# Kernel tuning notes

Measured on AMD Instinct MI355X. Metric: run time of the kernel, lower is better.

The kernel has to match this reference:

```python
import jax, jax.numpy as jnp
import numpy as np

B, N, C = 16, 2048, 512
NUM_HEADS = 8
D = C // NUM_HEADS  # 64


def setup_inputs() -> dict:
    key = jax.random.key(0)
    ks = jax.random.split(key, 8)
    s = 0.02
    return {
        "x": jax.random.normal(ks[0], (B, N, C), dtype=jnp.float32),
        "Wq": jax.random.normal(ks[1], (D, C), dtype=jnp.float32) * s,
        "bq": jax.random.normal(ks[2], (D,), dtype=jnp.float32) * s,
        "Wk": jax.random.normal(ks[3], (D, C), dtype=jnp.float32) * s,
        "bk": jax.random.normal(ks[4], (D,), dtype=jnp.float32) * s,
        "Wv": jax.random.normal(ks[5], (C, C), dtype=jnp.float32) * s,
        "bv": jax.random.normal(ks[6], (C,), dtype=jnp.float32) * s,
        "gamma": jax.random.normal(ks[7], (1,), dtype=jnp.float32) * 0.1,
    }


def reference(x, Wq, bq, Wk, bk, Wv, bv, gamma):
    # x: [B, N, C]; torch code permutes to [B, C, N] (channels for Conv1d)
    xt = jnp.transpose(x, (0, 2, 1))                      # [B, C, N]
    # 1x1 Conv1d == pointwise linear over channel dim
    q = jnp.einsum('dc,bcn->bdn', Wq, xt) + bq[None, :, None]   # [B, D, N]
    k = jnp.einsum('dc,bcn->bdn', Wk, xt) + bk[None, :, None]   # [B, D, N]
    v = jnp.einsum('oc,bcn->bon', Wv, xt) + bv[None, :, None]   # [B, C, N]
    # energy[b, n, m] = <q[:, n], k[:, m]>
    energy = jnp.einsum('bdn,bdm->bnm', q, k)             # [B, N, N]
    attention = jax.nn.softmax(energy, axis=-1)           # [B, N, N]
    # out = bmm(v, attention^T): out[b, c, n] = sum_m v[b, c, m] * attn[b, n, m]
    out = jnp.einsum('bcm,bnm->bcn', v, attention)        # [B, C, N]
    out = gamma[0] * out + xt
    return jnp.transpose(out, (0, 2, 1))                  # [B, N, C]
```

## Files before the change

### kernel.cpp

```cpp
#include <hip/hip_runtime.h>
#include <hip/hip_bf16.h>

typedef __bf16 bf16x8 __attribute__((ext_vector_type(8)));
typedef float f32x4 __attribute__((ext_vector_type(4)));

#define B_ 16
#define N_ 2048
#define C_ 512
#define D_ 64

__device__ __forceinline__ float bf2f(ushort u) {
    union { uint i; float f; } w; w.i = ((uint)u) << 16; return w.f;
}
__device__ __forceinline__ ushort f2bf(float f) {
    union { float f; uint i; } w; w.f = f;
    uint u = w.i;
    u = (u + 0x7fffu + ((u >> 16) & 1u)) >> 16;
    return (ushort)u;
}
__device__ __forceinline__ __bf16 u2b(ushort u) {
    union { ushort s; __bf16 b; } w; w.s = u; return w.b;
}
__device__ __forceinline__ bf16x8 ld8u(const ushort* p) { return *(const bf16x8*)p; }
__device__ __forceinline__ bf16x8 ld8f(const float* p) {
    f32x4 a = *(const f32x4*)p;
    f32x4 b = *(const f32x4*)(p + 4);
    bf16x8 r;
    r[0] = u2b(f2bf(a[0])); r[1] = u2b(f2bf(a[1]));
    r[2] = u2b(f2bf(a[2])); r[3] = u2b(f2bf(a[3]));
    r[4] = u2b(f2bf(b[0])); r[5] = u2b(f2bf(b[1]));
    r[6] = u2b(f2bf(b[2])); r[7] = u2b(f2bf(b[3]));
    return r;
}

__device__ __forceinline__ void gload16(const ushort* g, ushort* l) {
    __builtin_amdgcn_global_load_lds(
        (const __attribute__((address_space(1))) void*)g,
        (__attribute__((address_space(3))) void*)l, 16, 0, 0);
}

__global__ void probe_kernel(const void* x, int* flag) {
    int lane = threadIdx.x & 63;
    ushort u = ((const ushort*)x)[lane * 2];
    float v = fabsf(bf2f(u));
    bool sane = (v > 9.3e-10f) && (v < 1.1e9f) && (v == v);
    unsigned long long m = __ballot(sane);
    if (threadIdx.x == 0) *flag = (__popcll(m) >= 48) ? 0 : 1;
}

__launch_bounds__(256, 2)
__global__ void proj_all(const void* __restrict__ X,
                         const void* __restrict__ Wq_, const void* __restrict__ bq_,
                         const void* __restrict__ Wk_, const void* __restrict__ bk_,
                         const void* __restrict__ Wv_, const void* __restrict__ bv_,
                         ushort* __restrict__ outq,
                         ushort* __restrict__ outk,
                         ushort* __restrict__ outv,
                         const int* __restrict__ flag) {
    const int isf32 = *flag;
    __shared__ ushort lA[128][72];
    __shared__ ushort lB[128][72];
    const int tid  = threadIdx.x;
    const int wave = tid >> 6, lane = tid & 63;
    const int quad = lane >> 4, li = lane & 15;
    const int wr = (wave & 1) * 64;
    const int wc = (wave >> 1) * 64;
    const int m0 = blockIdx.x * 128;
    const int n0 = blockIdx.y * 128;

    f32x4 acc[4][4];
    #pragma unroll
    for (int i = 0; i < 4; ++i)
        #pragma unroll
        for (int j = 0; j < 4; ++j) acc[i][j] = (f32x4){0.f, 0.f, 0.f, 0.f};

    for (int k0 = 0; k0 < C_; k0 += 64) {
        __syncthreads();
        #pragma unroll
        for (int it = 0; it < 4; ++it) {
            int idx = tid + it * 256;
            int row = idx >> 3, seg = idx & 7;
            int n = n0 + row;
            size_t ea = (size_t)(m0 + row) * C_ + k0 + seg * 8;
            if (!isf32) {
                const ushort* bs = (n < 64)  ? (const ushort*)Wq_ + (size_t)n * C_
                                 : (n < 128) ? (const ushort*)Wk_ + (size_t)(n - 64) * C_
                                             : (const ushort*)Wv_ + (size_t)(n - 128) * C_;
                *(bf16x8*)&lA[row][seg * 8] = ld8u((const ushort*)X + ea);
                *(bf16x8*)&lB[row][seg * 8] = ld8u(bs + k0 + seg * 8);
            } else {
                const float* bs = (n < 64)  ? (const float*)Wq_ + (size_t)n * C_
                                : (n < 128) ? (const float*)Wk_ + (size_t)(n - 64) * C_
                                            : (const float*)Wv_ + (size_t)(n - 128) * C_;
                *(bf16x8*)&lA[row][seg * 8] = ld8f((const float*)X + ea);
                *(bf16x8*)&lB[row][seg * 8] = ld8f(bs + k0 + seg * 8);
            }
        }
        __syncthreads();
        #pragma unroll
        for (int ks = 0; ks < 2; ++ks) {
            bf16x8 af[4], bfr[4];
            #pragma unroll
            for (int i = 0; i < 4; ++i)
                af[i] = *(const bf16x8*)&lA[wr + i * 16 + li][ks * 32 + quad * 8];
            #pragma unroll
            for (int j = 0; j < 4; ++j)
                bfr[j] = *(const bf16x8*)&lB[wc + j * 16 + li][ks * 32 + quad * 8];
            #pragma unroll
            for (int i = 0; i < 4; ++i)
                #pragma unroll
                for (int j = 0; j < 4; ++j)
                    acc[i][j] = __builtin_amdgcn_mfma_f32_16x16x32_bf16(
                        af[i], bfr[j], acc[i][j], 0, 0, 0);
        }
    }

    #pragma unroll
    for (int j2 = 0; j2 < 4; ++j2) {
        int c = n0 + wc + j2 * 16 + li;
        float bv;
        if (!isf32) {
            bv = (c < 64)  ? bf2f(((const ushort*)bq_)[c])
               : (c < 128) ? bf2f(((const ushort*)bk_)[c - 64])
                           : bf2f(((const ushort*)bv_)[c - 128]);
        } else {
            bv = (c < 64)  ? ((const float*)bq_)[c]
               : (c < 128) ? ((const float*)bk_)[c - 64]
                           : ((const float*)bv_)[c - 128];
        }
        if (c < 128) {
            ushort* dst = (c < 64) ? outq : outk;
            int cl = c & 63;
            #pragma unroll
            for (int i = 0; i < 4; ++i)
                #pragma unroll
                for (int j = 0; j < 4; ++j) {
                    int m = m0 + wr + i * 16 + quad * 4 + j;
                    dst[(size_t)m * D_ + cl] = f2bf(acc[i][j2][j] + bv);
                }
        } else {
            int cv = c - 128;
            #pragma unroll
            for (int i = 0; i < 4; ++i) {
                int m = m0 + wr + i * 16 + quad * 4;
                int b = m >> 11, ml = m & (N_ - 1);
                ushort4 pk;
                pk.x = f2bf(acc[i][j2][0] + bv);
                pk.y = f2bf(acc[i][j2][1] + bv);
                pk.z = f2bf(acc[i][j2][2] + bv);
                pk.w = f2bf(acc[i][j2][3] + bv);
                *(ushort4*)(outv + ((size_t)(b * C_ + cv)) * N_ + ml) = pk;
            }
        }
    }
}

__launch_bounds__(512, 4)
__global__ void attn_fused(const ushort* __restrict__ q,
                           const ushort* __restrict__ kk,
                           const ushort* __restrict__ vt,
                           const void* __restrict__ x,
                           const void* __restrict__ gptr,
                           void* __restrict__ out,
                           const int* __restrict__ flag) {
    __shared__ ushort Vl[2][256 * 64];
    __shared__ ushort Pl[64 * 64];
    __shared__ float  ll[64];

    const int tid  = threadIdx.x;
    const int wave = tid >> 6, lane = tid & 63;
    const int quad = lane >> 4, li = lane & 15;
    const int wq = wave & 1;
    const int wm = wave >> 1;
    const int b  = blockIdx.z;
    const int q0 = blockIdx.x * 64;
    const int c0 = blockIdx.y * 256;

    const ushort* kb = kk + (size_t)b * N_ * D_;
    const ushort* vb = vt + ((size_t)b * C_ + c0) * N_;

    const int lrow8 = lane >> 3;
    const int lseg  = (lane & 7) ^ lrow8;

    bf16x8 qf[2][2];
    #pragma unroll
    for (int i = 0; i < 2; ++i)
        #pragma unroll
        for (int ks = 0; ks < 2; ++ks)
            qf[i][ks] = ld8u(q + ((size_t)(b * N_ + q0 + wq * 32 + i * 16 + li)) * D_
                               + ks * 32 + quad * 8);

    f32x4 acc[2][4];
    #pragma unroll
    for (int i = 0; i < 2; ++i)
        #pragma unroll
        for (int j = 0; j < 4; ++j) acc[i][j] = (f32x4){0.f, 0.f, 0.f, 0.f};

    f32x4 accp[2];
    float s4[2][4];
    #pragma unroll
    for (int i = 0; i < 2; ++i) {
        accp[i] = (f32x4){0.f, 0.f, 0.f, 0.f};
        #pragma unroll
        for (int j = 0; j < 4; ++j) s4[i][j] = 0.f;
    }

    #pragma unroll
    for (int it = 0; it < 4; ++it) {
        int rbase = wave * 32 + it * 8;
        gload16(vb + (size_t)(rbase + lrow8) * N_ + lseg * 8, &Vl[0][rbase * 64]);
    }
    {
        bf16x8 k0 = ld8u(kb + (size_t)(wm * 16 + li) * D_ + quad * 8);
        bf16x8 k1 = ld8u(kb + (size_t)(wm * 16 + li) * D_ + 32 + quad * 8);
        accp[0] = __builtin_amdgcn_mfma_f32_16x16x32_bf16(qf[0][0], k0, accp[0], 0, 0, 0);
        accp[1] = __builtin_amdgcn_mfma_f32_16x16x32_bf16(qf[1][0], k0, accp[1], 0, 0, 0);
        accp[0] = __builtin_amdgcn_mfma_f32_16x16x32_bf16(qf[0][1], k1, accp[0], 0, 0, 0);
        accp[1] = __builtin_amdgcn_mfma_f32_16x16x32_bf16(qf[1][1], k1, accp[1], 0, 0, 0);
    }
    bf16x8 kreg0 = ld8u(kb + (size_t)(64 + wm * 16 + li) * D_ + quad * 8);
    bf16x8 kreg1 = ld8u(kb + (size_t)(64 + wm * 16 + li) * D_ + 32 + quad * 8);

    for (int t = 0; t < 32; ++t) {
        const int cur = t & 1;
        if (t < 31) {
            #pragma unroll
            for (int it = 0; it < 4; ++it) {
                int rbase = wave * 32 + it * 8;
                gload16(vb + (size_t)(rbase + lrow8) * N_ + (t + 1) * 64 + lseg * 8,
                        &Vl[cur ^ 1][rbase * 64]);
            }
        }
        #pragma unroll
        for (int i = 0; i < 2; ++i)
            #pragma unroll
            for (int j = 0; j < 4; ++j) {
                int r = wq * 32 + i * 16 + quad * 4 + j;
                int m = wm * 16 + li;
                float e = __expf(fminf(accp[i][j], 60.f));
                s4[i][j] += e;
                *(__bf16*)&Pl[r * 64 + (((m >> 3) ^ (r & 7)) * 8) + (m & 7)] = (__bf16)e;
            }
        if (t < 31) {
            f32x4 np0 = (f32x4){0.f, 0.f, 0.f, 0.f};
            f32x4 np1 = (f32x4){0.f, 0.f, 0.f, 0.f};
            np0 = __builtin_amdgcn_mfma_f32_16x16x32_bf16(qf[0][0], kreg0, np0, 0, 0, 0);
            np1 = __builtin_amdgcn_mfma_f32_16x16x32_bf16(qf[1][0], kreg0, np1, 0, 0, 0);
            np0 = __builtin_amdgcn_mfma_f32_16x16x32_bf16(qf[0][1], kreg1, np0, 0, 0, 0);
            np1 = __builtin_amdgcn_mfma_f32_16x16x32_bf16(qf[1][1], kreg1, np1, 0, 0, 0);
            if (t < 30) {
                kreg0 = ld8u(kb + (size_t)((t + 2) * 64 + wm * 16 + li) * D_ + quad * 8);
                kreg1 = ld8u(kb + (size_t)((t + 2) * 64 + wm * 16 + li) * D_ + 32 + quad * 8);
            }
            accp[0] = np0;
            accp[1] = np1;
        }
        if (t < 30)       asm volatile("s_waitcnt vmcnt(6) lgkmcnt(0)" ::: "memory");
        else if (t == 30) asm volatile("s_waitcnt vmcnt(4) lgkmcnt(0)" ::: "memory");
        else              asm volatile("s_waitcnt vmcnt(0) lgkmcnt(0)" ::: "memory");
        __builtin_amdgcn_sched_barrier(0);
        __builtin_amdgcn_s_barrier();
        __builtin_amdgcn_sched_barrier(0);

        __builtin_amdgcn_s_setprio(1);
        #pragma unroll
        for (int ks = 0; ks < 2; ++ks) {
            bf16x8 af[2];
            #pragma unroll
            for (int i = 0; i < 2; ++i)
                af[i] = *(const bf16x8*)&Pl[(wq * 32 + i * 16 + li) * 64
                                            + (((ks * 4 + quad) ^ (li & 7)) * 8)];
            #pragma unroll
            for (int j = 0; j < 4; ++j) {
                bf16x8 vf = *(const bf16x8*)&Vl[cur][(wm * 64 + j * 16 + li) * 64
                                                    + (((ks * 4 + quad) ^ (li & 7)) * 8)];
                #pragma unroll
                for (int i = 0; i < 2; ++i)
                    acc[i][j] = __builtin_amdgcn_mfma_f32_16x16x32_bf16(
                        af[i], vf, acc[i][j], 0, 0, 0);
            }
        }
        __builtin_amdgcn_s_setprio(0);

        __builtin_amdgcn_sched_barrier(0);
        __builtin_amdgcn_s_barrier();
        __builtin_amdgcn_sched_barrier(0);
    }

    __syncthreads();
    if (tid < 64) ll[tid] = 0.f;
    __syncthreads();
    #pragma unroll
    for (int i = 0; i < 2; ++i)
        #pragma unroll
        for (int j = 0; j < 4; ++j) {
            float s = s4[i][j];
            s += __shfl_xor(s, 1, 64);
            s += __shfl_xor(s, 2, 64);
            s += __shfl_xor(s, 4, 64);
            s += __shfl_xor(s, 8, 64);
            if (li == 0) atomicAdd(&ll[wq * 32 + i * 16 + quad * 4 + j], s);
        }
    __syncthreads();

    const int isf32 = *flag;
    const float g = isf32 ? ((const float*)gptr)[0] : bf2f(((const ushort*)gptr)[0]);
    const ushort* xu = (const ushort*)x;
    const float*  xf = (const float*)x;
    ushort* ou = (ushort*)out;
    float*  of = (float*)out;
    #pragma unroll
    for (int i = 0; i < 2; ++i)
        #pragma unroll
        for (int jj = 0; jj < 4; ++jj) {
            int nl = wq * 32 + i * 16 + quad * 4 + jj;
            float inv = 1.f / ll[nl];
            size_t rowb = ((size_t)(b * N_ + q0 + nl)) * C_;
            #pragma unroll
            for (int j = 0; j < 4; ++j) {
                int cg = c0 + wm * 64 + j * 16 + li;
                size_t idx = rowb + cg;
                float xv  = isf32 ? xf[idx] : bf2f(xu[idx]);
                float val = g * (acc[i][j][jj] * inv) + xv;
                if (isf32) of[idx] = val; else ou[idx] = f2bf(val);
            }
        }
}

extern "C" void kernel_launch(void* const* d_in, const int* in_sizes, int n_in,
                              void* d_out, int out_size, void* d_ws, size_t ws_size,
                              hipStream_t stream) {
    (void)in_sizes; (void)n_in; (void)out_size; (void)ws_size;
    const void* x     = d_in[0];
    const void* Wq    = d_in[1];
    const void* bq    = d_in[2];
    const void* Wk    = d_in[3];
    const void* bk    = d_in[4];
    const void* Wv    = d_in[5];
    const void* bv    = d_in[6];
    const void* gamma = d_in[7];

    int*    flag = (int*)d_ws;
    ushort* q    = (ushort*)((char*)d_ws + 256);
    ushort* kk   = q  + (size_t)B_ * N_ * D_;
    ushort* vt   = kk + (size_t)B_ * N_ * D_;

    probe_kernel<<<1, 64, 0, stream>>>(x, flag);

    proj_all<<<dim3(B_ * N_ / 128, 640 / 128), 256, 0, stream>>>(
        x, Wq, bq, Wk, bk, Wv, bv, q, kk, vt, flag);

    attn_fused<<<dim3(N_ / 64, 2, B_), 512, 0, stream>>>(
        q, kk, vt, x, gamma, d_out, flag);
}
```

Baseline: 303.8 us.

## Pre-convert inputs to bf16 and stream projection tiles via direct global-to-LDS loads

Adds a separate conversion kernel that writes x and the stacked Q/K/V weights to bf16 in workspace. The projection GEMM can then fetch its tiles with global_load_lds into an XOR-swizzled LDS layout, instead of going through registers with per-element fp32 conversion. The grid is also transposed so the five N-tiles sharing one x row-block are adjacent, which should help L2 reuse of x. The cost is an extra full pass over x (read fp32, write bf16) plus more workspace.

```diff
diff --git a/kernel.cpp b/kernel.cpp
--- a/kernel.cpp
+++ b/kernel.cpp
@@ -48,25 +48,55 @@
     if (threadIdx.x == 0) *flag = (__popcll(m) >= 48) ? 0 : 1;
 }
 
+__global__ void convert_kernel(const void* __restrict__ X,
+                               const void* __restrict__ Wq_,
+                               const void* __restrict__ Wk_,
+                               const void* __restrict__ Wv_,
+                               ushort* __restrict__ xbf,
+                               ushort* __restrict__ wall,
+                               const int* __restrict__ flag) {
+    const int isf32 = *flag;
+    const size_t NX  = (size_t)B_ * N_ * C_;
+    const size_t NWQ = (size_t)D_ * C_;
+    const size_t NWV = (size_t)C_ * C_;
+    const size_t total8 = (NX + 2 * NWQ + NWV) / 8;
+    const size_t stride = (size_t)gridDim.x * blockDim.x;
+    for (size_t v = (size_t)blockIdx.x * blockDim.x + threadIdx.x; v < total8; v += stride) {
+        size_t e = v * 8;
+        const void* src;
+        size_t off;
+        ushort* dst;
+        if (e < NX)                { src = X;   off = e;                dst = xbf + e; }
+        else if (e < NX + NWQ)     { src = Wq_; off = e - NX;           dst = wall + (e - NX); }
+        else if (e < NX + 2 * NWQ) { src = Wk_; off = e - NX - NWQ;     dst = wall + (e - NX); }
+        else                       { src = Wv_; off = e - NX - 2 * NWQ; dst = wall + (e - NX); }
+        bf16x8 r = isf32 ? ld8f((const float*)src + off) : ld8u((const ushort*)src + off);
+        *(bf16x8*)dst = r;
+    }
+}
+
 __launch_bounds__(256, 2)
-__global__ void proj_all(const void* __restrict__ X,
-                         const void* __restrict__ Wq_, const void* __restrict__ bq_,
-                         const void* __restrict__ Wk_, const void* __restrict__ bk_,
-                         const void* __restrict__ Wv_, const void* __restrict__ bv_,
+__global__ void proj_all(const ushort* __restrict__ xbf,
+                         const ushort* __restrict__ wall,
+                         const void* __restrict__ bq_,
+                         const void* __restrict__ bk_,
+                         const void* __restrict__ bv_,
                          ushort* __restrict__ outq,
                          ushort* __restrict__ outk,
                          ushort* __restrict__ outv,
                          const int* __restrict__ flag) {
-    const int isf32 = *flag;
-    __shared__ ushort lA[128][72];
-    __shared__ ushort lB[128][72];
+    __shared__ ushort lA[128 * 64];
+    __shared__ ushort lB[128 * 64];
     const int tid  = threadIdx.x;
     const int wave = tid >> 6, lane = tid & 63;
     const int quad = lane >> 4, li = lane & 15;
     const int wr = (wave & 1) * 64;
     const int wc = (wave >> 1) * 64;
-    const int m0 = blockIdx.x * 128;
-    const int n0 = blockIdx.y * 128;
+    const int n0 = blockIdx.x * 128;
+    const int m0 = blockIdx.y * 128;
+
+    const int lrow8 = lane >> 3;
+    const int lseg  = (lane & 7) ^ (lrow8 & 7);
 
     f32x4 acc[4][4];
     #pragma unroll
@@ -77,35 +107,27 @@
     for (int k0 = 0; k0 < C_; k0 += 64) {
         __syncthreads();
         #pragma unroll
-        for (int it = 0; it < 4; ++it) {
-            int idx = tid + it * 256;
-            int row = idx >> 3, seg = idx & 7;
-            int n = n0 + row;
-            size_t ea = (size_t)(m0 + row) * C_ + k0 + seg * 8;
-            if (!isf32) {
-                const ushort* bs = (n < 64)  ? (const ushort*)Wq_ + (size_t)n * C_
-                                 : (n < 128) ? (const ushort*)Wk_ + (size_t)(n - 64) * C_
-                                             : (const ushort*)Wv_ + (size_t)(n - 128) * C_;
-                *(bf16x8*)&lA[row][seg * 8] = ld8u((const ushort*)X + ea);
-                *(bf16x8*)&lB[row][seg * 8] = ld8u(bs + k0 + seg * 8);
-            } else {
-                const float* bs = (n < 64)  ? (const float*)Wq_ + (size_t)n * C_
-                                : (n < 128) ? (const float*)Wk_ + (size_t)(n - 64) * C_
-                                            : (const float*)Wv_ + (size_t)(n - 128) * C_;
-                *(bf16x8*)&lA[row][seg * 8] = ld8f((const float*)X + ea);
-                *(bf16x8*)&lB[row][seg * 8] = ld8f(bs + k0 + seg * 8);
-            }
+        for (int i = 0; i < 4; ++i) {
+            int rbase = wave * 32 + i * 8;
+            gload16(xbf  + (size_t)(m0 + rbase + lrow8) * C_ + k0 + lseg * 8,
+                    &lA[rbase * 64]);
+            gload16(wall + (size_t)(n0 + rbase + lrow8) * C_ + k0 + lseg * 8,
+                    &lB[rbase * 64]);
         }
         __syncthreads();
         #pragma unroll
         for (int ks = 0; ks < 2; ++ks) {
             bf16x8 af[4], bfr[4];
             #pragma unroll
-            for (int i = 0; i < 4; ++i)
-                af[i] = *(const bf16x8*)&lA[wr + i * 16 + li][ks * 32 + quad * 8];
-            #pragma unroll
-            for (int j = 0; j < 4; ++j)
-                bfr[j] = *(const bf16x8*)&lB[wc + j * 16 + li][ks * 32 + quad * 8];
+            for (int i = 0; i < 4; ++i) {
+                int row = wr + i * 16 + li;
+                af[i] = *(const bf16x8*)&lA[row * 64 + (((ks * 4 + quad) ^ (li & 7)) * 8)];
+            }
+            #pragma unroll
+            for (int j = 0; j < 4; ++j) {
+                int row = wc + j * 16 + li;
+                bfr[j] = *(const bf16x8*)&lB[row * 64 + (((ks * 4 + quad) ^ (li & 7)) * 8)];
+            }
             #pragma unroll
             for (int i = 0; i < 4; ++i)
                 #pragma unroll
@@ -115,6 +137,7 @@
         }
     }
 
+    const int isf32 = *flag;
     #pragma unroll
     for (int j2 = 0; j2 < 4; ++j2) {
         int c = n0 + wc + j2 * 16 + li;
@@ -342,13 +365,16 @@
 
     int*    flag = (int*)d_ws;
     ushort* q    = (ushort*)((char*)d_ws + 256);
-    ushort* kk   = q  + (size_t)B_ * N_ * D_;
-    ushort* vt   = kk + (size_t)B_ * N_ * D_;
+    ushort* kk   = q   + (size_t)B_ * N_ * D_;
+    ushort* vt   = kk  + (size_t)B_ * N_ * D_;
+    ushort* xbf  = vt  + (size_t)B_ * C_ * N_;
+    ushort* wall = xbf + (size_t)B_ * N_ * C_;
 
     probe_kernel<<<1, 64, 0, stream>>>(x, flag);
-
-    proj_all<<<dim3(B_ * N_ / 128, 640 / 128), 256, 0, stream>>>(
-        x, Wq, bq, Wk, bk, Wv, bv, q, kk, vt, flag);
+    convert_kernel<<<2048, 256, 0, stream>>>(x, Wq, Wk, Wv, xbf, wall, flag);
+
+    proj_all<<<dim3(640 / 128, B_ * N_ / 128), 256, 0, stream>>>(
+        xbf, wall, bq, bk, bv, q, kk, vt, flag);
 
     attn_fused<<<dim3(N_ / 64, 2, B_), 512, 0, stream>>>(
         q, kk, vt, x, gamma, d_out, flag);
```

Result: faster. 292.5 us (-3.7%).
